# Performance work log

Measured on AMD Instinct MI355X. Metric: run time of the kernel, lower is better.

## Reference

```python
import jax, jax.numpy as jnp
import numpy as np

B, S, D = 2, 4096, 512
H = 8
HD = D // H


def setup_inputs() -> dict:
    key = jax.random.key(0)
    k1, k2, k3, k4, k5 = jax.random.split(key, 5)
    sd = 1.0 / np.sqrt(D)
    return {
        "x": jax.random.normal(k1, (B, S, D), dtype=jnp.float32),
        "Wqkv": jax.random.normal(k2, (3 * D, D), dtype=jnp.float32) * sd,
        "bqkv": jax.random.normal(k3, (3 * D,), dtype=jnp.float32) * 0.02,
        "Wo": jax.random.normal(k4, (D, D), dtype=jnp.float32) * sd,
        "bo": jax.random.normal(k5, (D,), dtype=jnp.float32) * 0.02,
    }


def reference(x, Wqkv, bqkv, Wo, bo):
    b, s, d = x.shape
    h, hd = H, d // H
    # QKV projection (torch Linear: x @ W^T + b)
    qkv = x @ Wqkv.T + bqkv                      # [b, s, 3d]
    q, k, v = jnp.split(qkv, 3, axis=-1)         # each [b, s, d]
    # [b, s, h, hd] -> [b, h, s, hd]
    q = q.reshape(b, s, h, hd).transpose(0, 2, 1, 3)
    k = k.reshape(b, s, h, hd).transpose(0, 2, 1, 3)
    v = v.reshape(b, s, h, hd).transpose(0, 2, 1, 3)
    # causal additive mask: triu(ones, diag=1) * -1e10
    mask = jnp.triu(jnp.ones((s, s), dtype=x.dtype), k=1) * jnp.asarray(-1e10, x.dtype)
    wts = jnp.einsum("bhqd,bhkd->bhqk", q, k) / np.sqrt(hd).astype(np.float32)
    wts = wts + mask[None, None, :, :]
    wts = jax.nn.softmax(wts, axis=-1)
    y = jnp.einsum("bhqk,bhkd->bhqd", wts, v)    # [b, h, s, hd]
    y = y.transpose(0, 2, 1, 3).reshape(b, s, d) # [b, s, d]
    out = y @ Wo.T + bo
    return out
```

## Files before the change

kernel.cpp:

```cpp
#include <hip/hip_runtime.h>


typedef __bf16 bf16x8 __attribute__((ext_vector_type(8)));
typedef float f32x4 __attribute__((ext_vector_type(4)));
typedef unsigned short u16;

#define MFMA(a, b, c) __builtin_amdgcn_mfma_f32_16x16x32_bf16(a, b, c, 0, 0, 0)
#define QSCALE 0.18033688011112042f

__device__ __forceinline__ float exp2_fast(float x) {
    return __builtin_amdgcn_exp2f(x);
}
__device__ __forceinline__ u16 f2bf(float f) {
    union { __bf16 h; u16 u; } v; v.h = (__bf16)f; return v.u;
}
__device__ __forceinline__ ushort4 f4_to_bf4(float4 v) {
    ushort4 r;
    r.x = f2bf(v.x); r.y = f2bf(v.y); r.z = f2bf(v.z); r.w = f2bf(v.w);
    return r;
}
__device__ __forceinline__ void load_lds16(const u16* g, u16* l) {
    __builtin_amdgcn_global_load_lds(
        (const __attribute__((address_space(1))) void*)g,
        (__attribute__((address_space(3))) void*)l, 16, 0, 0);
}

__global__ __launch_bounds__(256) void cvt_all(
    const float* __restrict__ x, const float* __restrict__ wq,
    const float* __restrict__ wo,
    u16* __restrict__ xb, u16* __restrict__ wqb, u16* __restrict__ wob)
{
    int i = blockIdx.x * 256 + threadIdx.x;
    if (i < 1048576) {
        ((ushort4*)xb)[i] = f4_to_bf4(((const float4*)x)[i]);
    } else if (i < 1048576 + 196608) {
        int j = i - 1048576;
        ((ushort4*)wqb)[j] = f4_to_bf4(((const float4*)wq)[j]);
    } else {
        int j = i - 1048576 - 196608;
        ((ushort4*)wob)[j] = f4_to_bf4(((const float4*)wo)[j]);
    }
}

__global__ __launch_bounds__(256) void gemm_qkv_bf(
    const u16* __restrict__ X, const u16* __restrict__ W,
    const float* __restrict__ bias,
    u16* __restrict__ QY, u16* __restrict__ Kf, u16* __restrict__ Vf)
{
    __shared__ u16 As[2 * 128 * 32];
    __shared__ u16 Bs[2 * 128 * 32];
    const int K = 512;
    const int tid = threadIdx.x, wave = tid >> 6, lane = tid & 63;
    const int l15 = lane & 15, quad = lane >> 4;
    const int bm = blockIdx.x * 128, bn = blockIdx.y * 128;
    const bool vmode = (bn >= 1024);
    const int wr = wave >> 1, wc = wave & 1;
    const int arow = lane >> 2;
    const int acol = (lane & 3) * 8;

    f32x4 acc[4][4] = {};
#pragma unroll
    for (int ii = 0; ii < 2; ii++) {
        const int inst = wave * 2 + ii;
        const int row = inst * 16 + arow;
        load_lds16(&X[(bm + row) * K + acol], &As[inst * 512]);
        load_lds16(&W[(bn + row) * K + acol], &Bs[inst * 512]);
    }
    int cur = 0;
    for (int k0 = 0; k0 < K; k0 += 32) {
        __builtin_amdgcn_s_barrier();
        if (k0 + 32 < K) {
            const int nb = (cur ^ 1) * 4096;
#pragma unroll
            for (int ii = 0; ii < 2; ii++) {
                const int inst = wave * 2 + ii;
                const int row = inst * 16 + arow;
                load_lds16(&X[(bm + row) * K + k0 + 32 + acol], &As[nb + inst * 512]);
                load_lds16(&W[(bn + row) * K + k0 + 32 + acol], &Bs[nb + inst * 512]);
            }
            asm volatile("s_waitcnt vmcnt(4)" ::: "memory");
        } else {
            asm volatile("s_waitcnt vmcnt(0)" ::: "memory");
        }
        __builtin_amdgcn_s_barrier();
        const int cb = cur * 4096;
        bf16x8 a[4], b[4];
#pragma unroll
        for (int i = 0; i < 4; i++)
            a[i] = *(const bf16x8*)&As[cb + (wr * 64 + i * 16 + l15) * 32 + quad * 8];
#pragma unroll
        for (int j = 0; j < 4; j++)
            b[j] = *(const bf16x8*)&Bs[cb + (wc * 64 + j * 16 + l15) * 32 + quad * 8];
        if (vmode) {
#pragma unroll
            for (int i = 0; i < 4; i++)
#pragma unroll
                for (int j = 0; j < 4; j++)
                    acc[i][j] = MFMA(a[j], b[i], acc[i][j]);
        } else {
#pragma unroll
            for (int i = 0; i < 4; i++)
#pragma unroll
                for (int j = 0; j < 4; j++)
                    acc[i][j] = MFMA(b[i], a[j], acc[i][j]);
        }
        cur ^= 1;
    }

    const int nbase = bn + wc * 64;
    if (vmode) {
#pragma unroll
        for (int i = 0; i < 4; i++) {
            const int d0 = nbase + i * 16 + l15;
            const float bvf = bias[d0];
            const int d0m = d0 & 511;
            const int h = d0m >> 6, hd0 = d0m & 63;
            const int n = hd0 >> 4, lv = hd0 & 15;
#pragma unroll
            for (int j = 0; j < 4; j++) {
                const int s_g = bm + wr * 64 + j * 16 + quad * 4;
                const int b_ = s_g >> 12, s0 = s_g & 4095;
                const int kt = s0 >> 6, kk = s0 & 63;
                const int half = kk >> 5, qv = (kk >> 3) & 3, e0 = kk & 7;
                ushort4 pk;
                pk.x = f2bf(acc[i][j][0] + bvf);
                pk.y = f2bf(acc[i][j][1] + bvf);
                pk.z = f2bf(acc[i][j][2] + bvf);
                pk.w = f2bf(acc[i][j][3] + bvf);
                const size_t off = ((size_t)((b_ * 8 + h) * 64 + kt)) * 4096 +
                                   n * 1024 + half * 512 + qv * 128 + lv * 8 + e0;
                *(ushort4*)&Vf[off] = pk;
            }
        }
    } else {
        const int which = nbase >> 9;
#pragma unroll
        for (int i = 0; i < 4; i++) {
            const int d0 = nbase + i * 16 + quad * 4;
            const float4 bv = *(const float4*)&bias[d0];
            const int d0m = d0 & 511;
            const int h = d0m >> 6, hd0 = d0m & 63;
#pragma unroll
            for (int j = 0; j < 4; j++) {
                const int s_g = bm + wr * 64 + j * 16 + l15;
                const int b_ = s_g >> 12, s0 = s_g & 4095;
                const int bhh = b_ * 8 + h;
                const int kt = s0 >> 6;
                if (which == 1) {
                    const int jj = (s0 >> 4) & 3, lr = s0 & 15;
                    const int half = hd0 >> 5, q4 = (hd0 >> 3) & 3, e0 = hd0 & 7;
                    ushort4 pk;
                    pk.x = f2bf(acc[i][j][0] + bv.x);
                    pk.y = f2bf(acc[i][j][1] + bv.y);
                    pk.z = f2bf(acc[i][j][2] + bv.z);
                    pk.w = f2bf(acc[i][j][3] + bv.w);
                    const size_t off = ((size_t)(bhh * 64 + kt)) * 4096 +
                                       jj * 1024 + half * 512 + q4 * 128 + lr * 8 + e0;
                    *(ushort4*)&Kf[off] = pk;
                } else {
                    ushort4 pk;
                    pk.x = f2bf((acc[i][j][0] + bv.x) * QSCALE);
                    pk.y = f2bf((acc[i][j][1] + bv.y) * QSCALE);
                    pk.z = f2bf((acc[i][j][2] + bv.z) * QSCALE);
                    pk.w = f2bf((acc[i][j][3] + bv.w) * QSCALE);
                    *(ushort4*)&QY[((b_ * 4096 + s0) * 8 + h) * 64 + hd0] = pk;
                }
            }
        }
    }
}

#define LS 72

#define GLD(dst, base, OFF)                                                  \
    asm volatile("global_load_dwordx4 %0, %1, off offset:" #OFF              \
                 : "=v"(dst) : "v"(base))

#define WAITV(N) do {                                                        \
    asm volatile("s_waitcnt vmcnt(" #N ")" ::: "memory");                    \
    __builtin_amdgcn_sched_barrier(0);                                       \
} while (0)

__global__ __launch_bounds__(128, 2) void attn_k(
    u16* __restrict__ QY, const u16* __restrict__ Kf, const u16* __restrict__ Vf)
{
    __shared__ u16 Ps[2 * 16 * LS];
    __shared__ float OxA[4][64][4];
    __shared__ float OxB[4][64][4];
    __shared__ float Lx[64][2];

    const int tid = threadIdx.x;
    const int wave = tid >> 6, lane = tid & 63;
    const int l15 = lane & 15, quad = lane >> 4;
    const int bh = blockIdx.x;
    const int b_ = bh >> 3, h = bh & 7;
    const int p = (int)blockIdx.y;
    const int seg = wave;

    bf16x8 ones;
#pragma unroll
    for (int i = 0; i < 8; i++) ones[i] = (__bf16)1.0f;

    const u16* KfB = &Kf[((size_t)bh * 64) * 4096 + lane * 8];
    const u16* VfB = &Vf[((size_t)bh * 64) * 4096 + lane * 8];
    u16* P = &Ps[wave * 16 * LS];

#define LOADK(DK, KT) do {                                                   \
    const u16* ka_ = KfB + (size_t)(KT) * 4096;                              \
    const u16* kb_ = ka_ + 2048;                                             \
    GLD(DK[0][0], ka_, 0);    GLD(DK[0][1], ka_, 1024);                      \
    GLD(DK[1][0], ka_, 2048); GLD(DK[1][1], ka_, 3072);                      \
    GLD(DK[2][0], kb_, 0);    GLD(DK[2][1], kb_, 1024);                      \
    GLD(DK[3][0], kb_, 2048); GLD(DK[3][1], kb_, 3072);                      \
} while (0)

#define LOADV(DV, KT) do {                                                   \
    const u16* va_ = VfB + (size_t)(KT) * 4096;                              \
    const u16* vb_ = va_ + 2048;                                             \
    GLD(DV[0][0], va_, 0);    GLD(DV[0][1], va_, 1024);                      \
    GLD(DV[1][0], va_, 2048); GLD(DV[1][1], va_, 3072);                      \
    GLD(DV[2][0], vb_, 0);    GLD(DV[2][1], vb_, 1024);                      \
    GLD(DV[3][0], vb_, 2048); GLD(DV[3][1], vb_, 3072);                      \
} while (0)

#define TILE_A(KC, KT) do {                                                  \
    const int k0_ = (KT) * 64;                                               \
    const bool nmA_ = (k0_ + 63 > base_r);                                   \
    const bool nmB_ = (k0_ + 63 > base_r + 16);                              \
    f32x4 sa_[4], sb_[4];                                                    \
    _Pragma("unroll")                                                        \
    for (int j_ = 0; j_ < 4; j_++) {                                         \
        f32x4 ia_ = {}, ib_ = {};                                            \
        if (nmA_) {                                                          \
            _Pragma("unroll")                                                \
            for (int r_ = 0; r_ < 4; r_++) {                                 \
                const int key_ = k0_ + j_ * 16 + quad * 4 + r_;              \
                ia_[r_] = (key_ > rowA) ? -1e30f : 0.0f;                     \
            }                                                                \
        }                                                                    \
        if (nmB_) {                                                          \
            _Pragma("unroll")                                                \
            for (int r_ = 0; r_ < 4; r_++) {                                 \
                const int key_ = k0_ + j_ * 16 + quad * 4 + r_;              \
                ib_[r_] = (key_ > rowA + 16) ? -1e30f : 0.0f;                \
            }                                                                \
        }                                                                    \
        ia_ = MFMA(KC[j_][0], qa0, ia_);                                     \
        sa_[j_] = MFMA(KC[j_][1], qa1, ia_);                                 \
        ib_ = MFMA(KC[j_][0], qb0, ib_);                                     \
        sb_[j_] = MFMA(KC[j_][1], qb1, ib_);                                 \
    }                                                                        \
    _Pragma("unroll")                                                        \
    for (int j_ = 0; j_ < 4; j_++) {                                         \
        ushort4 w_;                                                          \
        w_.x = f2bf(exp2_fast(sa_[j_][0]));                                  \
        w_.y = f2bf(exp2_fast(sa_[j_][1]));                                  \
        w_.z = f2bf(exp2_fast(sa_[j_][2]));                                  \
        w_.w = f2bf(exp2_fast(sa_[j_][3]));                                  \
        *(ushort4*)&P[l15 * LS + j_ * 16 + quad * 4] = w_;                   \
    }                                                                        \
    _Pragma("unroll")                                                        \
    for (int j_ = 0; j_ < 4; j_++)                                           \
        _Pragma("unroll")                                                    \
        for (int r_ = 0; r_ < 4; r_++)                                       \
            spb[j_][r_] = exp2_fast(sb_[j_][r_]);                            \
    pfa0 = *(const bf16x8*)&P[l15 * LS + quad * 8];                          \
    pfa1 = *(const bf16x8*)&P[l15 * LS + 32 + quad * 8];                     \
    _Pragma("unroll")                                                        \
    for (int j_ = 0; j_ < 4; j_++) {                                         \
        ushort4 w_;                                                          \
        w_.x = f2bf(spb[j_][0]); w_.y = f2bf(spb[j_][1]);                    \
        w_.z = f2bf(spb[j_][2]); w_.w = f2bf(spb[j_][3]);                    \
        *(ushort4*)&P[l15 * LS + j_ * 16 + quad * 4] = w_;                   \
    }                                                                        \
} while (0)

#define TILE_B(VC) do {                                                      \
    lacc_a = MFMA(ones, pfa0, lacc_a);                                       \
    lacc_a = MFMA(ones, pfa1, lacc_a);                                       \
    _Pragma("unroll")                                                        \
    for (int n_ = 0; n_ < 4; n_++) {                                         \
        oa[n_] = MFMA(VC[n_][0], pfa0, oa[n_]);                              \
        oa[n_] = MFMA(VC[n_][1], pfa1, oa[n_]);                              \
    }                                                                        \
    bf16x8 pfb0_ = *(const bf16x8*)&P[l15 * LS + quad * 8];                  \
    bf16x8 pfb1_ = *(const bf16x8*)&P[l15 * LS + 32 + quad * 8];             \
    lacc_b = MFMA(ones, pfb0_, lacc_b);                                      \
    lacc_b = MFMA(ones, pfb1_, lacc_b);                                      \
    _Pragma("unroll")                                                        \
    for (int n_ = 0; n_ < 4; n_++) {                                         \
        ob[n_] = MFMA(VC[n_][0], pfb0_, ob[n_]);                             \
        ob[n_] = MFMA(VC[n_][1], pfb1_, ob[n_]);                             \
    }                                                                        \
} while (0)

    for (int phase = 0; phase < 2; phase++) {
        const int qt32 = phase ? (127 - p) : p;
        const int nt = (qt32 >> 1) + 1;
        const int hlf = (nt + 1) >> 1;
        const int t0 = seg ? hlf : 0;
        const int t1 = seg ? nt : hlf;
        const int base_r = qt32 * 32;

        const u16* qpa = &QY[((b_ * 4096 + base_r + l15) * 8 + h) * 64 + quad * 8];
        const u16* qpb = qpa + 16 * 8 * 64;
        bf16x8 qa0, qa1, qb0, qb1;
        GLD(qa0, qpa, 0);
        GLD(qa1, qpa, 64);
        GLD(qb0, qpb, 0);
        GLD(qb1, qpb, 64);

        f32x4 oa[4] = {}, ob[4] = {};
        f32x4 lacc_a = {}, lacc_b = {};
        const int rowA = base_r + l15;

        float spb[4][4];
        bf16x8 pfa0, pfa1;
        bf16x8 kR[4][2], kS[4][2], vv[4][2];

        if (t0 < t1) LOADK(kR, t0);
        for (int kt = t0; kt < t1; kt += 2) {
            const bool h1 = (kt + 1 < t1);
            LOADV(vv, kt);
            if (h1) LOADK(kS, kt + 1);
            if (h1) { WAITV(16); } else { WAITV(8); }
            TILE_A(kR, kt);
            if (h1) { WAITV(8); } else { WAITV(0); }
            TILE_B(vv);
            if (h1) {
                const bool h2 = (kt + 2 < t1);
                LOADV(vv, kt + 1);
                if (h2) LOADK(kR, kt + 2);
                if (h2) { WAITV(16); } else { WAITV(8); }
                TILE_A(kS, kt + 1);
                if (h2) { WAITV(8); } else { WAITV(0); }
                TILE_B(vv);
            }
        }

        if (wave == 1) {
#pragma unroll
            for (int n = 0; n < 4; n++) {
                *(f32x4*)&OxA[n][lane][0] = oa[n];
                *(f32x4*)&OxB[n][lane][0] = ob[n];
            }
            Lx[lane][0] = lacc_a[0];
            Lx[lane][1] = lacc_b[0];
        }
        __syncthreads();
        if (wave == 0) {
            const float la = lacc_a[0] + Lx[lane][0];
            const float lb = lacc_b[0] + Lx[lane][1];
            const float iva = (la > 0.0f) ? 1.0f / la : 0.0f;
            const float ivb = (lb > 0.0f) ? 1.0f / lb : 0.0f;
            u16* ya = &QY[((size_t)((b_ * 4096 + base_r + l15) * 8 + h)) * 64];
            u16* yb = ya + 16 * 8 * 64;
#pragma unroll
            for (int n = 0; n < 4; n++) {
                f32x4 sa4 = *(const f32x4*)&OxA[n][lane][0];
                f32x4 sb4 = *(const f32x4*)&OxB[n][lane][0];
                ushort4 wa;
                wa.x = f2bf((oa[n][0] + sa4[0]) * iva);
                wa.y = f2bf((oa[n][1] + sa4[1]) * iva);
                wa.z = f2bf((oa[n][2] + sa4[2]) * iva);
                wa.w = f2bf((oa[n][3] + sa4[3]) * iva);
                *(ushort4*)&ya[n * 16 + quad * 4] = wa;
                ushort4 wb;
                wb.x = f2bf((ob[n][0] + sb4[0]) * ivb);
                wb.y = f2bf((ob[n][1] + sb4[1]) * ivb);
                wb.z = f2bf((ob[n][2] + sb4[2]) * ivb);
                wb.w = f2bf((ob[n][3] + sb4[3]) * ivb);
                *(ushort4*)&yb[n * 16 + quad * 4] = wb;
            }
        }
        __syncthreads();
    }
#undef LOADK
#undef LOADV
#undef TILE_A
#undef TILE_B
}

__global__ __launch_bounds__(256) void gemm_o_bf(
    const u16* __restrict__ X, const u16* __restrict__ W,
    const float* __restrict__ bias, float* __restrict__ Out)
{
    __shared__ u16 As[2 * 128 * 32];
    __shared__ u16 Bs[2 * 128 * 32];
    const int K = 512;
    const int tid = threadIdx.x, wave = tid >> 6, lane = tid & 63;
    const int l15 = lane & 15, quad = lane >> 4;
    const int bm = blockIdx.x * 128, bn = blockIdx.y * 128;
    const int wr = wave >> 1, wc = wave & 1;
    const int arow = lane >> 2;
    const int acol = (lane & 3) * 8;

    f32x4 acc[4][4] = {};
#pragma unroll
    for (int ii = 0; ii < 2; ii++) {
        const int inst = wave * 2 + ii;
        const int row = inst * 16 + arow;
        load_lds16(&X[(bm + row) * K + acol], &As[inst * 512]);
        load_lds16(&W[(bn + row) * K + acol], &Bs[inst * 512]);
    }
    int cur = 0;
    for (int k0 = 0; k0 < K; k0 += 32) {
        __builtin_amdgcn_s_barrier();
        if (k0 + 32 < K) {
            const int nb = (cur ^ 1) * 4096;
#pragma unroll
            for (int ii = 0; ii < 2; ii++) {
                const int inst = wave * 2 + ii;
                const int row = inst * 16 + arow;
                load_lds16(&X[(bm + row) * K + k0 + 32 + acol], &As[nb + inst * 512]);
                load_lds16(&W[(bn + row) * K + k0 + 32 + acol], &Bs[nb + inst * 512]);
            }
            asm volatile("s_waitcnt vmcnt(4)" ::: "memory");
        } else {
            asm volatile("s_waitcnt vmcnt(0)" ::: "memory");
        }
        __builtin_amdgcn_s_barrier();
        const int cb = cur * 4096;
        bf16x8 a[4], b[4];
#pragma unroll
        for (int i = 0; i < 4; i++)
            a[i] = *(const bf16x8*)&As[cb + (wr * 64 + i * 16 + l15) * 32 + quad * 8];
#pragma unroll
        for (int j = 0; j < 4; j++)
            b[j] = *(const bf16x8*)&Bs[cb + (wc * 64 + j * 16 + l15) * 32 + quad * 8];
#pragma unroll
        for (int i = 0; i < 4; i++)
#pragma unroll
            for (int j = 0; j < 4; j++)
                acc[i][j] = MFMA(b[i], a[j], acc[i][j]);
        cur ^= 1;
    }
#pragma unroll
    for (int i = 0; i < 4; i++) {
        const int n0 = bn + wc * 64 + i * 16 + quad * 4;
        const float4 bv = *(const float4*)&bias[n0];
#pragma unroll
        for (int j = 0; j < 4; j++) {
            const int m = bm + wr * 64 + j * 16 + l15;
            float4 ov;
            ov.x = acc[i][j][0] + bv.x;
            ov.y = acc[i][j][1] + bv.y;
            ov.z = acc[i][j][2] + bv.z;
            ov.w = acc[i][j][3] + bv.w;
            *(float4*)&Out[(size_t)m * 512 + n0] = ov;
        }
    }
}

extern "C" void kernel_launch(void* const* d_in, const int* in_sizes, int n_in,
                              void* d_out, int out_size, void* d_ws, size_t ws_size,
                              hipStream_t stream) {
    (void)in_sizes; (void)n_in; (void)out_size; (void)ws_size;
    const float* x    = (const float*)d_in[0];
    const float* Wqkv = (const float*)d_in[1];
    const float* bqkv = (const float*)d_in[2];
    const float* Wo   = (const float*)d_in[3];
    const float* bo   = (const float*)d_in[4];
    float* out = (float*)d_out;

    u16* qy_ws = (u16*)d_ws;
    u16* kf_ws = qy_ws + 4194304;
    u16* vf_ws = kf_ws + 4194304;
    float* ml  = (float*)(vf_ws + 4194304);
    u16* wqkvb = (u16*)(ml + 262144);
    u16* wob   = wqkvb + 786432;
    u16* xb    = (u16*)d_out;

    cvt_all<<<5120, 256, 0, stream>>>(x, Wqkv, Wo, xb, wqkvb, wob);
    gemm_qkv_bf<<<dim3(64, 12), 256, 0, stream>>>(xb, wqkvb, bqkv, qy_ws, kf_ws, vf_ws);
    attn_k<<<dim3(16, 64), 128, 0, stream>>>(qy_ws, kf_ws, vf_ws);
    gemm_o_bf<<<dim3(64, 4), 256, 0, stream>>>(qy_ws, wob, bo, out);
}
```

Before: 174.3 us.

## Shrink attention query tile from 32 to 16 rows and double grid

```diff
diff --git a/kernel.cpp b/kernel.cpp
--- a/kernel.cpp
+++ b/kernel.cpp
@@ -186,8 +186,7 @@
 {
     __shared__ u16 Ps[2 * 16 * LS];
     __shared__ float OxA[4][64][4];
-    __shared__ float OxB[4][64][4];
-    __shared__ float Lx[64][2];
+    __shared__ float Lx[64];
 
     const int tid = threadIdx.x;
     const int wave = tid >> 6, lane = tid & 63;
@@ -226,11 +225,10 @@
 #define TILE_A(KC, KT) do {                                                  \
     const int k0_ = (KT) * 64;                                               \
     const bool nmA_ = (k0_ + 63 > base_r);                                   \
-    const bool nmB_ = (k0_ + 63 > base_r + 16);                              \
-    f32x4 sa_[4], sb_[4];                                                    \
+    f32x4 sa_[4];                                                            \
     _Pragma("unroll")                                                        \
     for (int j_ = 0; j_ < 4; j_++) {                                         \
-        f32x4 ia_ = {}, ib_ = {};                                            \
+        f32x4 ia_ = {};                                                      \
         if (nmA_) {                                                          \
             _Pragma("unroll")                                                \
             for (int r_ = 0; r_ < 4; r_++) {                                 \
@@ -238,17 +236,8 @@
                 ia_[r_] = (key_ > rowA) ? -1e30f : 0.0f;                     \
             }                                                                \
         }                                                                    \
-        if (nmB_) {                                                          \
-            _Pragma("unroll")                                                \
-            for (int r_ = 0; r_ < 4; r_++) {                                 \
-                const int key_ = k0_ + j_ * 16 + quad * 4 + r_;              \
-                ib_[r_] = (key_ > rowA + 16) ? -1e30f : 0.0f;                \
-            }                                                                \
-        }                                                                    \
         ia_ = MFMA(KC[j_][0], qa0, ia_);                                     \
         sa_[j_] = MFMA(KC[j_][1], qa1, ia_);                                 \
-        ib_ = MFMA(KC[j_][0], qb0, ib_);                                     \
-        sb_[j_] = MFMA(KC[j_][1], qb1, ib_);                                 \
     }                                                                        \
     _Pragma("unroll")                                                        \
     for (int j_ = 0; j_ < 4; j_++) {                                         \
@@ -259,20 +248,8 @@
         w_.w = f2bf(exp2_fast(sa_[j_][3]));                                  \
         *(ushort4*)&P[l15 * LS + j_ * 16 + quad * 4] = w_;                   \
     }                                                                        \
-    _Pragma("unroll")                                                        \
-    for (int j_ = 0; j_ < 4; j_++)                                           \
-        _Pragma("unroll")                                                    \
-        for (int r_ = 0; r_ < 4; r_++)                                       \
-            spb[j_][r_] = exp2_fast(sb_[j_][r_]);                            \
     pfa0 = *(const bf16x8*)&P[l15 * LS + quad * 8];                          \
     pfa1 = *(const bf16x8*)&P[l15 * LS + 32 + quad * 8];                     \
-    _Pragma("unroll")                                                        \
-    for (int j_ = 0; j_ < 4; j_++) {                                         \
-        ushort4 w_;                                                          \
-        w_.x = f2bf(spb[j_][0]); w_.y = f2bf(spb[j_][1]);                    \
-        w_.z = f2bf(spb[j_][2]); w_.w = f2bf(spb[j_][3]);                    \
-        *(ushort4*)&P[l15 * LS + j_ * 16 + quad * 4] = w_;                   \
-    }                                                                        \
 } while (0)
 
 #define TILE_B(VC) do {                                                      \
@@ -283,94 +260,71 @@
         oa[n_] = MFMA(VC[n_][0], pfa0, oa[n_]);                              \
         oa[n_] = MFMA(VC[n_][1], pfa1, oa[n_]);                              \
     }                                                                        \
-    bf16x8 pfb0_ = *(const bf16x8*)&P[l15 * LS + quad * 8];                  \
-    bf16x8 pfb1_ = *(const bf16x8*)&P[l15 * LS + 32 + quad * 8];             \
-    lacc_b = MFMA(ones, pfb0_, lacc_b);                                      \
-    lacc_b = MFMA(ones, pfb1_, lacc_b);                                      \
-    _Pragma("unroll")                                                        \
-    for (int n_ = 0; n_ < 4; n_++) {                                         \
-        ob[n_] = MFMA(VC[n_][0], pfb0_, ob[n_]);                             \
-        ob[n_] = MFMA(VC[n_][1], pfb1_, ob[n_]);                             \
-    }                                                                        \
 } while (0)
 
     for (int phase = 0; phase < 2; phase++) {
-        const int qt32 = phase ? (127 - p) : p;
-        const int nt = (qt32 >> 1) + 1;
+        const int qt16 = phase ? (255 - p) : p;
+        const int nt = (qt16 >> 2) + 1;
         const int hlf = (nt + 1) >> 1;
         const int t0 = seg ? hlf : 0;
         const int t1 = seg ? nt : hlf;
-        const int base_r = qt32 * 32;
-
-        const u16* qpa = &QY[((b_ * 4096 + base_r + l15) * 8 + h) * 64 + quad * 8];
-        const u16* qpb = qpa + 16 * 8 * 64;
-        bf16x8 qa0, qa1, qb0, qb1;
-        GLD(qa0, qpa, 0);
-        GLD(qa1, qpa, 64);
-        GLD(qb0, qpb, 0);
-        GLD(qb1, qpb, 64);
-
-        f32x4 oa[4] = {}, ob[4] = {};
-        f32x4 lacc_a = {}, lacc_b = {};
+        const int base_r = qt16 * 16;
+
+        f32x4 oa[4] = {};
+        f32x4 lacc_a = {};
         const int rowA = base_r + l15;
 
-        float spb[4][4];
-        bf16x8 pfa0, pfa1;
-        bf16x8 kR[4][2], kS[4][2], vv[4][2];
-
-        if (t0 < t1) LOADK(kR, t0);
-        for (int kt = t0; kt < t1; kt += 2) {
-            const bool h1 = (kt + 1 < t1);
-            LOADV(vv, kt);
-            if (h1) LOADK(kS, kt + 1);
-            if (h1) { WAITV(16); } else { WAITV(8); }
-            TILE_A(kR, kt);
-            if (h1) { WAITV(8); } else { WAITV(0); }
-            TILE_B(vv);
-            if (h1) {
-                const bool h2 = (kt + 2 < t1);
-                LOADV(vv, kt + 1);
-                if (h2) LOADK(kR, kt + 2);
-                if (h2) { WAITV(16); } else { WAITV(8); }
-                TILE_A(kS, kt + 1);
-                if (h2) { WAITV(8); } else { WAITV(0); }
+        if (t0 < t1) {
+            const u16* qpa = &QY[((b_ * 4096 + base_r + l15) * 8 + h) * 64 + quad * 8];
+            bf16x8 qa0, qa1;
+            GLD(qa0, qpa, 0);
+            GLD(qa1, qpa, 64);
+
+            bf16x8 pfa0, pfa1;
+            bf16x8 kR[4][2], kS[4][2], vv[4][2];
+
+            LOADK(kR, t0);
+            for (int kt = t0; kt < t1; kt += 2) {
+                const bool h1 = (kt + 1 < t1);
+                LOADV(vv, kt);
+                if (h1) LOADK(kS, kt + 1);
+                if (h1) { WAITV(16); } else { WAITV(8); }
+                TILE_A(kR, kt);
+                if (h1) { WAITV(8); } else { WAITV(0); }
                 TILE_B(vv);
-            }
+                if (h1) {
+                    const bool h2 = (kt + 2 < t1);
+                    LOADV(vv, kt + 1);
+                    if (h2) LOADK(kR, kt + 2);
+                    if (h2) { WAITV(16); } else { WAITV(8); }
+                    TILE_A(kS, kt + 1);
+                    if (h2) { WAITV(8); } else { WAITV(0); }
+                    TILE_B(vv);
+                }
+            }
+            WAITV(0);
         }
 
         if (wave == 1) {
 #pragma unroll
-            for (int n = 0; n < 4; n++) {
+            for (int n = 0; n < 4; n++)
                 *(f32x4*)&OxA[n][lane][0] = oa[n];
-                *(f32x4*)&OxB[n][lane][0] = ob[n];
-            }
-            Lx[lane][0] = lacc_a[0];
-            Lx[lane][1] = lacc_b[0];
+            Lx[lane] = lacc_a[0];
         }
         __syncthreads();
         if (wave == 0) {
-            const float la = lacc_a[0] + Lx[lane][0];
-            const float lb = lacc_b[0] + Lx[lane][1];
+            const float la = lacc_a[0] + Lx[lane];
             const float iva = (la > 0.0f) ? 1.0f / la : 0.0f;
-            const float ivb = (lb > 0.0f) ? 1.0f / lb : 0.0f;
             u16* ya = &QY[((size_t)((b_ * 4096 + base_r + l15) * 8 + h)) * 64];
-            u16* yb = ya + 16 * 8 * 64;
 #pragma unroll
             for (int n = 0; n < 4; n++) {
-                f32x4 sa4 = *(const f32x4*)&OxA[n][lane][0];
-                f32x4 sb4 = *(const f32x4*)&OxB[n][lane][0];
+                f32x4 s0 = *(const f32x4*)&OxA[n][lane][0];
                 ushort4 wa;
-                wa.x = f2bf((oa[n][0] + sa4[0]) * iva);
-                wa.y = f2bf((oa[n][1] + sa4[1]) * iva);
-                wa.z = f2bf((oa[n][2] + sa4[2]) * iva);
-                wa.w = f2bf((oa[n][3] + sa4[3]) * iva);
+                wa.x = f2bf((oa[n][0] + s0[0]) * iva);
+                wa.y = f2bf((oa[n][1] + s0[1]) * iva);
+                wa.z = f2bf((oa[n][2] + s0[2]) * iva);
+                wa.w = f2bf((oa[n][3] + s0[3]) * iva);
                 *(ushort4*)&ya[n * 16 + quad * 4] = wa;
-                ushort4 wb;
-                wb.x = f2bf((ob[n][0] + sb4[0]) * ivb);
-                wb.y = f2bf((ob[n][1] + sb4[1]) * ivb);
-                wb.z = f2bf((ob[n][2] + sb4[2]) * ivb);
-                wb.w = f2bf((ob[n][3] + sb4[3]) * ivb);
-                *(ushort4*)&yb[n * 16 + quad * 4] = wb;
             }
         }
         __syncthreads();
@@ -473,6 +427,6 @@
 
     cvt_all<<<5120, 256, 0, stream>>>(x, Wqkv, Wo, xb, wqkvb, wob);
     gemm_qkv_bf<<<dim3(64, 12), 256, 0, stream>>>(xb, wqkvb, bqkv, qy_ws, kf_ws, vf_ws);
-    attn_k<<<dim3(16, 64), 128, 0, stream>>>(qy_ws, kf_ws, vf_ws);
+    attn_k<<<dim3(16, 128), 128, 0, stream>>>(qy_ws, kf_ws, vf_ws);
     gemm_o_bf<<<dim3(64, 4), 256, 0, stream>>>(qy_ws, wob, bo, out);
 }
```

Result: slower. 195.9 us (+12.4%).
